# Kernel tuning notes

Measured on AMD Instinct MI355X. Metric: run time of the kernel, lower is better.

## Reference

```python
import jax, jax.numpy as jnp
import numpy as np

N, E, C_IN, H = 50000, 800000, 128, 128
BN_EPS = 1e-5


def gcn_conv(x, W, b, src, dst, n):
    # Dense transform then degree-normalized (GCN) neighbor aggregation with self-loops
    h = x @ W  # [N, H]
    deg = jax.ops.segment_sum(jnp.ones_like(dst, dtype=h.dtype), dst, num_segments=n)
    dinv = jax.lax.rsqrt(jnp.maximum(deg, 1.0))  # self-loops guarantee deg >= 1
    norm = dinv[src] * dinv[dst]                 # [E+N]
    msg = h[src] * norm[:, None]                 # gather + scale
    out = jax.ops.segment_sum(msg, dst, num_segments=n)  # scatter-add
    return out + b


def batchnorm(x, gamma, beta):
    mu = jnp.mean(x, axis=0)
    var = jnp.mean(jnp.square(x - mu), axis=0)  # biased var, as torch BN training
    return (x - mu) * jax.lax.rsqrt(var + BN_EPS) * gamma + beta


def setup_inputs() -> dict:
    key = jax.random.key(0)
    ks = jax.random.split(key, 8)
    node_feat = jax.random.normal(ks[0], (N, C_IN), dtype=jnp.float32)
    edge_index = jax.random.randint(ks[1], (2, E), 0, N, dtype=jnp.int64)
    s1 = 1.0 / np.sqrt(C_IN)
    s2 = 1.0 / np.sqrt(H)
    return {
        "node_feat": node_feat,
        "edge_index": edge_index,
        "W1": jax.random.uniform(ks[2], (C_IN, H), jnp.float32, -s1, s1),
        "b1": jnp.zeros((H,), jnp.float32),
        "W2": jax.random.uniform(ks[3], (H, H), jnp.float32, -s2, s2),
        "b2": jnp.zeros((H,), jnp.float32),
        "g1": jnp.ones((H,), jnp.float32),
        "beta1": jnp.zeros((H,), jnp.float32),
        "g2": jnp.ones((H,), jnp.float32),
        "beta2": jnp.zeros((H,), jnp.float32),
    }


def reference(node_feat, edge_index, W1, b1, W2, b2, g1, beta1, g2, beta2):
    n = node_feat.shape[0]
    sl = jnp.arange(n, dtype=edge_index.dtype)
    src = jnp.concatenate([edge_index[0], sl])  # add self-loops
    dst = jnp.concatenate([edge_index[1], sl])
    x = jax.nn.relu(batchnorm(gcn_conv(node_feat, W1, b1, src, dst, n), g1, beta1))
    x = jax.nn.relu(batchnorm(gcn_conv(x, W2, b2, src, dst, n), g2, beta2))
    # dropout is identity in eval / deterministic reference
    return x
```

## Files before the change

### kernel.cpp

```cpp
#include <hip/hip_runtime.h>

__device__ __forceinline__ float b2f(unsigned short u) {
    union { unsigned int i; float f; } x; x.i = ((unsigned int)u) << 16; return x.f;
}
__device__ __forceinline__ unsigned short f2b(float f) {
    union { float f; unsigned int i; } x; x.f = f;
    unsigned int r = x.i + 0x7fffu + ((x.i >> 16) & 1u);
    return (unsigned short)(r >> 16);
}
__device__ __forceinline__ bool finitef(float x) {
    union { float f; unsigned int u; } c; c.f = x;
    return ((c.u >> 23) & 0xffu) != 0xffu;
}

typedef __attribute__((ext_vector_type(8))) __bf16 bf16x8;
typedef __attribute__((ext_vector_type(4))) float f32x4;

#define HDIM 128
#define LSTR 136
#define ROWU 64
#define DCAP 62
#define NCOPY 32
#define NB 256
#define BCAP 8192

__device__ __forceinline__ void bn_compute(const float* colsum, const float* colsq,
                                           const unsigned short* gam, const unsigned short* bet,
                                           int isbf, float invn, int f,
                                           float* sc_out, float* sf_out) {
    float cs = 0.f, cq = 0.f;
#pragma unroll
    for (int c = 0; c < NCOPY; ++c) {
        cs += colsum[c * 128 + f];
        cq += colsq[c * 128 + f];
    }
    float gv, bv;
    if (isbf) { gv = b2f(gam[f]);            bv = b2f(bet[f]); }
    else      { gv = ((const float*)gam)[f]; bv = ((const float*)bet)[f]; }
    if (!finitef(cs) || !finitef(cq)) { *sc_out = 0.f; *sf_out = 150.f; return; }
    float mu = cs * invn;
    float var = cq * invn - mu * mu;
    var = var < 0.f ? 0.f : var;
    float rstd = rsqrtf(var + 1e-5f);
    float s = gv * rstd;
    *sc_out = s;
    *sf_out = bv - mu * s;
}

__global__ void fill_f32(float* p, int n, float v) {
    int i = blockIdx.x * 256 + threadIdx.x;
    if (i < n) p[i] = v;
}

__global__ void prep(const unsigned short* __restrict__ X0, const int* __restrict__ ei,
                     const unsigned short* __restrict__ W1, const unsigned short* __restrict__ W2,
                     unsigned short* __restrict__ Wt1, unsigned short* __restrict__ Wt2,
                     int* __restrict__ zbase, int zcount, int* __restrict__ flags) {
    int bid = blockIdx.x, tid = threadIdx.x;
    if (bid < 128) {
        __shared__ int sane, hi64;
        if (tid == 0) { sane = 0; hi64 = 0; }
        __syncthreads();
        unsigned short u = X0[2 * tid];
        int e = (u >> 7) & 0xff;
        if (e >= 100 && e <= 140) atomicAdd(&sane, 1);
        if (bid == 0 && tid < 64) {
            if (ei[2 * tid + 1] != 0) atomicAdd(&hi64, 1);
        }
        __syncthreads();
        int isbf = (sane >= 128) ? 1 : 0;
        if (bid == 0 && tid == 0) { flags[0] = isbf; flags[1] = (hi64 == 0) ? 1 : 0; }
        int idx = bid * 256 + tid;
        const unsigned short* src; unsigned short* dst; int l;
        if (idx < 16384) { src = W1; dst = Wt1; l = idx; }
        else             { src = W2; dst = Wt2; l = idx - 16384; }
        int k = l >> 7, c = l & 127;
        unsigned short v = isbf ? src[l] : f2b(((const float*)src)[l]);
        dst[c * 128 + k] = v;
    } else {
        int i = (bid - 128) * 256 + tid;
        if (i < zcount) zbase[i] = 0;
    }
}

__global__ __launch_bounds__(256) void bin_edges(const int* __restrict__ ei,
                                                 unsigned int* __restrict__ bData,
                                                 unsigned int* __restrict__ bCnt,
                                                 const int* __restrict__ flags,
                                                 int E, int N, int BSZ) {
    __shared__ unsigned int cnt[NB];
    __shared__ unsigned int base[NB];
    int tid = threadIdx.x;
    int is64 = flags[1];
    int e0 = blockIdx.x * 4096;
    cnt[tid] = 0;
    __syncthreads();
    unsigned int val[16], loff[16]; int bk[16];
#pragma unroll
    for (int j = 0; j < 16; ++j) {
        int e = e0 + j * 256 + tid;
        bk[j] = -1;
        if (e < E) {
            int d, s;
            if (is64) { d = ei[2 * (size_t)E + 2 * (size_t)e]; s = ei[2 * (size_t)e]; }
            else      { d = ei[(size_t)E + e];                 s = ei[e]; }
            d = d < 0 ? 0 : (d >= N ? N - 1 : d);
            s = s < 0 ? 0 : (s >= N ? N - 1 : s);
            int b = d / BSZ;
            int loc = d - b * BSZ;
            val[j] = (unsigned int)s | ((unsigned int)loc << 16);
            bk[j] = b;
            loff[j] = atomicAdd(&cnt[b], 1u);
        }
    }
    __syncthreads();
    unsigned int c = cnt[tid];
    base[tid] = (c > 0) ? atomicAdd(&bCnt[tid], c) : 0u;
    __syncthreads();
#pragma unroll
    for (int j = 0; j < 16; ++j) {
        if (bk[j] >= 0) {
            unsigned int pos = base[bk[j]] + loff[j];
            if (pos < BCAP) bData[(size_t)bk[j] * BCAP + pos] = val[j];
        }
    }
}

__global__ __launch_bounds__(256) void build_csr(const unsigned int* __restrict__ bData,
                                                 const unsigned int* __restrict__ bCnt,
                                                 unsigned short* __restrict__ csr2d,
                                                 int N, int BSZ) {
    __shared__ __align__(16) unsigned short rows[256 * ROWU];
    int b = blockIdx.x;
    int tid = threadIdx.x;
    int node0 = b * BSZ;
    int nn = N - node0; if (nn > BSZ) nn = BSZ;
    if (nn <= 0) return;
    uint4* r4 = (uint4*)rows;
#pragma unroll
    for (int i = 0; i < 8; ++i) { uint4 z = {0u, 0u, 0u, 0u}; r4[tid + i * 256] = z; }
    __syncthreads();
    unsigned int ne = bCnt[b]; if (ne > BCAP) ne = BCAP;
    const unsigned int* bd = &bData[(size_t)b * BCAP];
    for (unsigned int t = tid; t < ne; t += 256) {
        unsigned int v = bd[t];
        unsigned int loc = v >> 16;
        unsigned int s = v & 0xffffu;
        unsigned int c = atomicAdd((unsigned int*)&rows[loc * ROWU], 1u);
        if (c < DCAP) rows[loc * ROWU + 2 + c] = (unsigned short)s;
    }
    __syncthreads();
    uint4* g4 = (uint4*)&csr2d[(size_t)node0 * ROWU];
    int tot = nn * (ROWU / 8);
    for (int i = tid; i < tot; i += 256) g4[i] = r4[i];
}

__global__ __launch_bounds__(256) void gemm_mfma(
    const unsigned short* __restrict__ A, const unsigned short* __restrict__ Wt,
    unsigned short* __restrict__ C, const int* __restrict__ aflag, int mode,
    const float* __restrict__ colsum, const float* __restrict__ colsq,
    const unsigned short* __restrict__ gam, const unsigned short* __restrict__ bet,
    float invn, const unsigned short* __restrict__ csr2d, int n) {
    __shared__ __align__(16) unsigned short Wl[128 * LSTR];
    __shared__ __align__(16) unsigned short Al[64 * LSTR];
    __shared__ float sc_sh[128], sf_sh[128];
    int tid = threadIdx.x;
    int row0 = blockIdx.x * 64;
    int isbf = aflag[0];

    if (mode == 2 && tid < 128)
        bn_compute(colsum, colsq, gam, bet, isbf, invn, tid, &sc_sh[tid], &sf_sh[tid]);

    const uint4* Wg = (const uint4*)Wt;
#pragma unroll
    for (int it = 0; it < 8; ++it) {
        int idx = tid + it * 256;
        int nn = idx >> 4, k8 = idx & 15;
        *(uint4*)&Wl[nn * LSTR + k8 * 8] = Wg[idx];
    }
    if (mode == 2) __syncthreads();

    int amode = (mode == 2) ? 2 : isbf;
    if (amode == 1) {
        const uint4* Ag = (const uint4*)A;
        for (int it = 0; it < 4; ++it) {
            int idx = tid + it * 256;
            int r = idx >> 4, cc = idx & 15;
            int gr = row0 + r;
            uint4 v; v.x = v.y = v.z = v.w = 0u;
            if (gr < n) v = Ag[(size_t)gr * 16 + cc];
            *(uint4*)&Al[r * LSTR + cc * 8] = v;
        }
    } else if (amode == 0) {
        const uint4* Af = (const uint4*)A;
        for (int it = 0; it < 8; ++it) {
            int idx = tid + it * 256;
            int r = idx >> 5, c4 = idx & 31;
            int gr = row0 + r;
            uint4 v; v.x = v.y = v.z = v.w = 0u;
            if (gr < n) v = Af[(size_t)gr * 32 + c4];
            float ff[4]; *(uint4*)ff = v;
            ushort4 o;
            o.x = f2b(ff[0]); o.y = f2b(ff[1]); o.z = f2b(ff[2]); o.w = f2b(ff[3]);
            *(ushort4*)&Al[r * LSTR + c4 * 4] = o;
        }
    } else {
        const uint4* Ag = (const uint4*)A;
        for (int it = 0; it < 4; ++it) {
            int idx = tid + it * 256;
            int r = idx >> 4, cc = idx & 15;
            int gr = row0 + r;
            uint4 v; v.x = v.y = v.z = v.w = 0u;
            if (gr < n) v = Ag[(size_t)gr * 16 + cc];
            unsigned short hu[8]; *(uint4*)hu = v;
            unsigned short ou[8];
#pragma unroll
            for (int j = 0; j < 8; ++j) {
                int f = cc * 8 + j;
                float x = b2f(hu[j]) * sc_sh[f] + sf_sh[f];
                ou[j] = f2b(x > 0.f ? x : 0.f);
            }
            *(uint4*)&Al[r * LSTR + cc * 8] = *(uint4*)ou;
        }
    }
    __syncthreads();

    int wave = tid >> 6, lane = tid & 63;
    int m = lane & 15, quad = lane >> 4;

    bf16x8 afr[4];
#pragma unroll
    for (int kc = 0; kc < 4; ++kc)
        afr[kc] = *(const bf16x8*)&Al[(wave * 16 + m) * LSTR + kc * 32 + quad * 8];

    float dv[4];
#pragma unroll
    for (int i2 = 0; i2 < 4; ++i2) {
        int gr = row0 + wave * 16 + quad * 4 + i2;
        if (gr < n) {
            int ct = *(const int*)&csr2d[(size_t)gr * ROWU];
            dv[i2] = rsqrtf((float)ct + 1.0f);
        } else dv[i2] = 0.f;
    }

    for (int t = 0; t < 8; ++t) {
        f32x4 acc = {0.f, 0.f, 0.f, 0.f};
#pragma unroll
        for (int kc = 0; kc < 4; ++kc) {
            bf16x8 bfr = *(const bf16x8*)&Wl[(t * 16 + m) * LSTR + kc * 32 + quad * 8];
            acc = __builtin_amdgcn_mfma_f32_16x16x32_bf16(afr[kc], bfr, acc, 0, 0, 0);
        }
#pragma unroll
        for (int i2 = 0; i2 < 4; ++i2) {
            int gr = row0 + wave * 16 + quad * 4 + i2;
            if (gr < n) C[(size_t)gr * 128 + t * 16 + m] = f2b(acc[i2] * dv[i2]);
        }
    }
}

__global__ __launch_bounds__(256) void agg_stats(
    const unsigned short* __restrict__ Hb, const unsigned short* __restrict__ csr2d,
    unsigned short* __restrict__ AGG,
    float* __restrict__ colsum, float* __restrict__ colsq, int n) {
    int tid = threadIdx.x;
    int wave = tid >> 6, lane = tid & 63;
    int g = lane >> 4, q = lane & 15;

    float s1[8], s2[8];
#pragma unroll
    for (int j = 0; j < 8; ++j) { s1[j] = 0.f; s2[j] = 0.f; }

    for (int i = blockIdx.x * 4 + wave; i < n; i += gridDim.x * 4) {
        const unsigned short* row = &csr2d[(size_t)i * ROWU];
        int ct = *(const int*)row;
        float di = rsqrtf((float)ct + 1.0f);
        int c = ct < DCAP ? ct : DCAP;
        const unsigned short* adj = row + 2;
        float acc[8];
#pragma unroll
        for (int j = 0; j < 8; ++j) acc[j] = 0.f;

        if (g == 0) {
            uint4 a4 = *(const uint4*)&Hb[(size_t)i * 128 + q * 8];
            unsigned short au[8]; *(uint4*)au = a4;
#pragma unroll
            for (int j = 0; j < 8; ++j) acc[j] += b2f(au[j]);
        }

        int t = g;
        for (; t + 12 < c; t += 16) {
            int sA = adj[t];
            int sB = adj[t + 4];
            int sC = adj[t + 8];
            int sD = adj[t + 12];
            uint4 a4 = *(const uint4*)&Hb[(size_t)sA * 128 + q * 8];
            uint4 b4 = *(const uint4*)&Hb[(size_t)sB * 128 + q * 8];
            uint4 c4 = *(const uint4*)&Hb[(size_t)sC * 128 + q * 8];
            uint4 d4 = *(const uint4*)&Hb[(size_t)sD * 128 + q * 8];
            unsigned short au[8]; *(uint4*)au = a4;
            unsigned short bu[8]; *(uint4*)bu = b4;
            unsigned short cu[8]; *(uint4*)cu = c4;
            unsigned short du[8]; *(uint4*)du = d4;
#pragma unroll
            for (int j = 0; j < 8; ++j)
                acc[j] += (b2f(au[j]) + b2f(bu[j])) + (b2f(cu[j]) + b2f(du[j]));
        }
        for (; t < c; t += 4) {
            int sA = adj[t];
            uint4 a4 = *(const uint4*)&Hb[(size_t)sA * 128 + q * 8];
            unsigned short au[8]; *(uint4*)au = a4;
#pragma unroll
            for (int j = 0; j < 8; ++j) acc[j] += b2f(au[j]);
        }

#pragma unroll
        for (int j = 0; j < 8; ++j) {
            acc[j] += __shfl_xor(acc[j], 16, 64);
            acc[j] += __shfl_xor(acc[j], 32, 64);
            acc[j] *= di;
        }
        if (g == 0) {
            unsigned short ou[8];
#pragma unroll
            for (int j = 0; j < 8; ++j) {
                float v = acc[j];
                ou[j] = f2b(v);
                s1[j] += v; s2[j] += v * v;
            }
            *(uint4*)&AGG[(size_t)i * 128 + q * 8] = *(uint4*)ou;
        }
    }

    __shared__ float sh[4][256];
    if (g == 0) {
#pragma unroll
        for (int j = 0; j < 8; ++j) {
            sh[wave][q * 8 + j] = s1[j];
            sh[wave][128 + q * 8 + j] = s2[j];
        }
    }
    __syncthreads();
    if (tid < 128) {
        float a = sh[0][tid] + sh[1][tid] + sh[2][tid] + sh[3][tid];
        float b = sh[0][128 + tid] + sh[1][128 + tid] + sh[2][128 + tid] + sh[3][128 + tid];
        int copy = blockIdx.x & (NCOPY - 1);
        atomicAdd(&colsum[copy * 128 + tid], a);
        atomicAdd(&colsq[copy * 128 + tid], b);
    }
}

__global__ void bn_apply_f32(const unsigned short* __restrict__ AGG,
                             const float* __restrict__ colsum, const float* __restrict__ colsq,
                             const unsigned short* __restrict__ gam, const unsigned short* __restrict__ bet,
                             const int* __restrict__ flag, float invn,
                             float* __restrict__ out, int nchunk) {
    __shared__ float sc_sh[128], sf_sh[128];
    int tid = threadIdx.x;
    if (tid < 128)
        bn_compute(colsum, colsq, gam, bet, flag[0], invn, tid, &sc_sh[tid], &sf_sh[tid]);
    __syncthreads();
    int i = blockIdx.x * 256 + tid;
    if (i >= nchunk) return;
    int base = i * 8;
    int f0 = base & 127;
    uint4 hv = *(const uint4*)&AGG[base];
    unsigned short hu[8]; *(uint4*)hu = hv;
    float o[8];
#pragma unroll
    for (int j = 0; j < 8; ++j) {
        float v = b2f(hu[j]) * sc_sh[f0 + j] + sf_sh[f0 + j];
        o[j] = v > 0.f ? v : 0.f;
    }
    *(float4*)&out[base] = *(float4*)&o[0];
    *(float4*)&out[base + 4] = *(float4*)&o[4];
}

extern "C" void kernel_launch(void* const* d_in, const int* in_sizes, int n_in,
                              void* d_out, int out_size, void* d_ws, size_t ws_size,
                              hipStream_t stream) {
    const unsigned short* X0 = (const unsigned short*)d_in[0];
    const int* ei = (const int*)d_in[1];
    const unsigned short* W1 = (const unsigned short*)d_in[2];
    const unsigned short* W2 = (const unsigned short*)d_in[4];
    const unsigned short* g1 = (const unsigned short*)d_in[6];
    const unsigned short* be1 = (const unsigned short*)d_in[7];
    const unsigned short* g2 = (const unsigned short*)d_in[8];
    const unsigned short* be2 = (const unsigned short*)d_in[9];
    float* OUT = (float*)d_out;

    int N = in_sizes[0] / HDIM;
    int E = in_sizes[1] / 2;
    int total = N * HDIM;
    int applyb = (total + 255) / 256;

    bool ok = (n_in == 10) && (N > 0) && (in_sizes[0] == N * HDIM) && (E > 0)
           && (in_sizes[2] == HDIM * HDIM) && (in_sizes[4] == HDIM * HDIM)
           && (in_sizes[6] == HDIM) && (in_sizes[9] == HDIM) && (out_size == total)
           && (N <= 65536);
    if (!ok) { fill_f32<<<applyb, 256, 0, stream>>>(OUT, total, -100.0f); return; }

    size_t need = 1024 + (size_t)N * ROWU * 2 + (size_t)NCOPY * 512 * 4 + NB * 4 + 64
                + (size_t)total * 4 + 65536 + (size_t)NB * BCAP * 4 + 4096;
    if (ws_size < need) { fill_f32<<<applyb, 256, 0, stream>>>(OUT, total, -300.0f); return; }

    char* w = (char*)d_ws;
    w = (char*)(((uintptr_t)w + 255) & ~(uintptr_t)255);
    unsigned short* csr2d = (unsigned short*)w; w += (size_t)N * ROWU * 2;
    float* stats = (float*)w; w += (size_t)NCOPY * 512 * 4;
    unsigned int* bCnt = (unsigned int*)w; w += NB * 4;
    int* flags = (int*)w;     w += 64;
    w = (char*)(((uintptr_t)w + 255) & ~(uintptr_t)255);
    unsigned short* Hb = (unsigned short*)w;  w += (size_t)total * 2;
    unsigned short* AGG = (unsigned short*)w; w += (size_t)total * 2;
    unsigned short* Wt1 = (unsigned short*)w; w += (size_t)HDIM * HDIM * 2;
    unsigned short* Wt2 = (unsigned short*)w; w += (size_t)HDIM * HDIM * 2;
    w = (char*)(((uintptr_t)w + 255) & ~(uintptr_t)255);
    unsigned int* bData = (unsigned int*)w; w += (size_t)NB * BCAP * 4;

    float* colsum1 = stats;
    float* colsq1 = stats + NCOPY * 128;
    float* colsum2 = stats + 2 * NCOPY * 128;
    float* colsq2 = stats + 3 * NCOPY * 128;

    int gemmb = (N + 63) / 64;
    float invn = 1.0f / (float)N;
    int BSZ = (N + NB - 1) / NB;
    int zcount = NCOPY * 512 + NB;

    prep<<<128 + (zcount + 255) / 256, 256, 0, stream>>>(X0, ei, W1, W2, Wt1, Wt2,
                                                         (int*)stats, zcount, flags);
    bin_edges<<<(E + 4095) / 4096, 256, 0, stream>>>(ei, bData, bCnt, flags, E, N, BSZ);
    build_csr<<<NB, 256, 0, stream>>>(bData, bCnt, csr2d, N, BSZ);

    gemm_mfma<<<gemmb, 256, 0, stream>>>(X0, Wt1, Hb, flags, -1,
                                         nullptr, nullptr, nullptr, nullptr, invn, csr2d, N);
    agg_stats<<<2048, 256, 0, stream>>>(Hb, csr2d, AGG, colsum1, colsq1, N);

    gemm_mfma<<<gemmb, 256, 0, stream>>>(AGG, Wt2, Hb, flags, 2,
                                         colsum1, colsq1, g1, be1, invn, csr2d, N);
    agg_stats<<<2048, 256, 0, stream>>>(Hb, csr2d, AGG, colsum2, colsq2, N);

    bn_apply_f32<<<(total / 8 + 255) / 256, 256, 0, stream>>>(AGG, colsum2, colsq2,
                                                              g2, be2, flags, invn, OUT, total / 8);
}
```

Measured before the change: 239.2 us.

## Split feature dim into two halves and map halves to XCD groups for cache locality

Stores intermediate H and AGG as two column-halves of 64 features each, laid out as [2][N][64]. Aggregation blocks are assigned to a half by XCD index (blockIdx & 7), so each group of XCDs gathers only half the feature matrix. The aim is to shrink each XCD's gather working set so it fits better in its L2. The trade-off is more edge-index reads per node and an extra shuffle stage, and correctness depends on the round-robin block-to-XCD mapping assumed for grid-size balance.

```diff
diff --git a/kernel.cpp b/kernel.cpp
--- a/kernel.cpp
+++ b/kernel.cpp
@@ -167,6 +167,7 @@
     int tid = threadIdx.x;
     int row0 = blockIdx.x * 64;
     int isbf = aflag[0];
+    size_t cs = (size_t)n * 64;
 
     if (mode == 2 && tid < 128)
         bn_compute(colsum, colsq, gam, bet, isbf, invn, tid, &sc_sh[tid], &sf_sh[tid]);
@@ -206,12 +207,13 @@
         }
     } else {
         const uint4* Ag = (const uint4*)A;
+        size_t cs4 = (size_t)n * 8;
         for (int it = 0; it < 4; ++it) {
             int idx = tid + it * 256;
             int r = idx >> 4, cc = idx & 15;
             int gr = row0 + r;
             uint4 v; v.x = v.y = v.z = v.w = 0u;
-            if (gr < n) v = Ag[(size_t)gr * 16 + cc];
+            if (gr < n) v = Ag[(size_t)(cc >> 3) * cs4 + (size_t)gr * 8 + (cc & 7)];
             unsigned short hu[8]; *(uint4*)hu = v;
             unsigned short ou[8];
 #pragma unroll
@@ -250,10 +252,12 @@
             bf16x8 bfr = *(const bf16x8*)&Wl[(t * 16 + m) * LSTR + kc * 32 + quad * 8];
             acc = __builtin_amdgcn_mfma_f32_16x16x32_bf16(afr[kc], bfr, acc, 0, 0, 0);
         }
+        unsigned short* Cb = C + (size_t)(t >> 2) * cs;
+        int fl = (t & 3) * 16 + m;
 #pragma unroll
         for (int i2 = 0; i2 < 4; ++i2) {
             int gr = row0 + wave * 16 + quad * 4 + i2;
-            if (gr < n) C[(size_t)gr * 128 + t * 16 + m] = f2b(acc[i2] * dv[i2]);
+            if (gr < n) Cb[(size_t)gr * 64 + fl] = f2b(acc[i2] * dv[i2]);
         }
     }
 }
@@ -263,14 +267,22 @@
     unsigned short* __restrict__ AGG,
     float* __restrict__ colsum, float* __restrict__ colsq, int n) {
     int tid = threadIdx.x;
+    int bid = blockIdx.x;
     int wave = tid >> 6, lane = tid & 63;
-    int g = lane >> 4, q = lane & 15;
+    int g = lane >> 3, q = lane & 7;
+    int xcd = bid & 7;
+    int half = xcd >> 2;
+    int sb = (bid >> 3) * 4 + (xcd & 3);
+    int gid = sb * 4 + wave;
+    int ngrp = (gridDim.x >> 3) * 16;
+    const unsigned short* Hh = Hb + (size_t)half * (size_t)n * 64;
+    unsigned short* Ah = AGG + (size_t)half * (size_t)n * 64;
 
     float s1[8], s2[8];
 #pragma unroll
     for (int j = 0; j < 8; ++j) { s1[j] = 0.f; s2[j] = 0.f; }
 
-    for (int i = blockIdx.x * 4 + wave; i < n; i += gridDim.x * 4) {
+    for (int i = gid; i < n; i += ngrp) {
         const unsigned short* row = &csr2d[(size_t)i * ROWU];
         int ct = *(const int*)row;
         float di = rsqrtf((float)ct + 1.0f);
@@ -281,33 +293,26 @@
         for (int j = 0; j < 8; ++j) acc[j] = 0.f;
 
         if (g == 0) {
-            uint4 a4 = *(const uint4*)&Hb[(size_t)i * 128 + q * 8];
+            uint4 a4 = *(const uint4*)&Hh[(size_t)i * 64 + q * 8];
             unsigned short au[8]; *(uint4*)au = a4;
 #pragma unroll
             for (int j = 0; j < 8; ++j) acc[j] += b2f(au[j]);
         }
 
         int t = g;
-        for (; t + 12 < c; t += 16) {
+        for (; t + 8 < c; t += 16) {
             int sA = adj[t];
-            int sB = adj[t + 4];
-            int sC = adj[t + 8];
-            int sD = adj[t + 12];
-            uint4 a4 = *(const uint4*)&Hb[(size_t)sA * 128 + q * 8];
-            uint4 b4 = *(const uint4*)&Hb[(size_t)sB * 128 + q * 8];
-            uint4 c4 = *(const uint4*)&Hb[(size_t)sC * 128 + q * 8];
-            uint4 d4 = *(const uint4*)&Hb[(size_t)sD * 128 + q * 8];
+            int sB = adj[t + 8];
+            uint4 a4 = *(const uint4*)&Hh[(size_t)sA * 64 + q * 8];
+            uint4 b4 = *(const uint4*)&Hh[(size_t)sB * 64 + q * 8];
             unsigned short au[8]; *(uint4*)au = a4;
             unsigned short bu[8]; *(uint4*)bu = b4;
-            unsigned short cu[8]; *(uint4*)cu = c4;
-            unsigned short du[8]; *(uint4*)du = d4;
-#pragma unroll
-            for (int j = 0; j < 8; ++j)
-                acc[j] += (b2f(au[j]) + b2f(bu[j])) + (b2f(cu[j]) + b2f(du[j]));
-        }
-        for (; t < c; t += 4) {
+#pragma unroll
+            for (int j = 0; j < 8; ++j) acc[j] += b2f(au[j]) + b2f(bu[j]);
+        }
+        for (; t < c; t += 8) {
             int sA = adj[t];
-            uint4 a4 = *(const uint4*)&Hb[(size_t)sA * 128 + q * 8];
+            uint4 a4 = *(const uint4*)&Hh[(size_t)sA * 64 + q * 8];
             unsigned short au[8]; *(uint4*)au = a4;
 #pragma unroll
             for (int j = 0; j < 8; ++j) acc[j] += b2f(au[j]);
@@ -315,6 +320,7 @@
 
 #pragma unroll
         for (int j = 0; j < 8; ++j) {
+            acc[j] += __shfl_xor(acc[j], 8, 64);
             acc[j] += __shfl_xor(acc[j], 16, 64);
             acc[j] += __shfl_xor(acc[j], 32, 64);
             acc[j] *= di;
@@ -327,25 +333,24 @@
                 ou[j] = f2b(v);
                 s1[j] += v; s2[j] += v * v;
             }
-            *(uint4*)&AGG[(size_t)i * 128 + q * 8] = *(uint4*)ou;
-        }
-    }
-
-    __shared__ float sh[4][256];
+            *(uint4*)&Ah[(size_t)i * 64 + q * 8] = *(uint4*)ou;
+        }
+    }
+
+    __shared__ float sh[4][128];
     if (g == 0) {
 #pragma unroll
         for (int j = 0; j < 8; ++j) {
             sh[wave][q * 8 + j] = s1[j];
-            sh[wave][128 + q * 8 + j] = s2[j];
+            sh[wave][64 + q * 8 + j] = s2[j];
         }
     }
     __syncthreads();
     if (tid < 128) {
         float a = sh[0][tid] + sh[1][tid] + sh[2][tid] + sh[3][tid];
-        float b = sh[0][128 + tid] + sh[1][128 + tid] + sh[2][128 + tid] + sh[3][128 + tid];
-        int copy = blockIdx.x & (NCOPY - 1);
-        atomicAdd(&colsum[copy * 128 + tid], a);
-        atomicAdd(&colsq[copy * 128 + tid], b);
+        int copy = bid & (NCOPY - 1);
+        if (tid < 64) atomicAdd(&colsum[copy * 128 + half * 64 + tid], a);
+        else          atomicAdd(&colsq[copy * 128 + half * 64 + (tid - 64)], a);
     }
 }
 
@@ -353,7 +358,7 @@
                              const float* __restrict__ colsum, const float* __restrict__ colsq,
                              const unsigned short* __restrict__ gam, const unsigned short* __restrict__ bet,
                              const int* __restrict__ flag, float invn,
-                             float* __restrict__ out, int nchunk) {
+                             float* __restrict__ out, int nchunk, int n) {
     __shared__ float sc_sh[128], sf_sh[128];
     int tid = threadIdx.x;
     if (tid < 128)
@@ -362,8 +367,10 @@
     int i = blockIdx.x * 256 + tid;
     if (i >= nchunk) return;
     int base = i * 8;
+    int node = base >> 7;
     int f0 = base & 127;
-    uint4 hv = *(const uint4*)&AGG[base];
+    size_t cs = (size_t)n * 64;
+    uint4 hv = *(const uint4*)&AGG[(size_t)(f0 >> 6) * cs + (size_t)node * 64 + (f0 & 63)];
     unsigned short hu[8]; *(uint4*)hu = hv;
     float o[8];
 #pragma unroll
@@ -441,5 +448,5 @@
     agg_stats<<<2048, 256, 0, stream>>>(Hb, csr2d, AGG, colsum2, colsq2, N);
 
     bn_apply_f32<<<(total / 8 + 255) / 256, 256, 0, stream>>>(AGG, colsum2, colsq2,
-                                                              g2, be2, flags, invn, OUT, total / 8);
-}
+                                                              g2, be2, flags, invn, OUT, total / 8, N);
+}
```

Result: slower. 265.5 us (+11.0%).
